# Optimization experiments

Measured on AMD Instinct MI355X. Metric: run time of the kernel, lower is better.

The kernel has to match this reference:

```python
import jax, jax.numpy as jnp
import numpy as np

MAX_DET = 100
IOU_THR = 0.5


def _iou_matrix(b):
    # b: [N,4] xyxy -> [N,N] pairwise IoU
    area = jnp.clip(b[:, 2] - b[:, 0], 0) * jnp.clip(b[:, 3] - b[:, 1], 0)
    lt = jnp.maximum(b[:, None, :2], b[None, :, :2])
    rb = jnp.minimum(b[:, None, 2:], b[None, :, 2:])
    wh = jnp.clip(rb - lt, 0)
    inter = wh[..., 0] * wh[..., 1]
    union = area[:, None] + area[None, :] - inter
    return inter / jnp.maximum(union, 1e-8)


def _batched_nms(boxes, scores, classes, iou_thr, max_out):
    # torchvision batched_nms semantics: offset boxes by class id so
    # boxes of different classes never overlap, then greedy NMS.
    n = boxes.shape[0]
    order = jnp.argsort(-scores)
    b = boxes[order]
    c = classes[order]
    off = c.astype(b.dtype) * (jnp.max(b) + 1.0)
    iou = _iou_matrix(b + off[:, None])  # [N,N]

    def body(valid, _):
        idx = jnp.argmax(valid)          # highest-score surviving candidate
        any_valid = jnp.any(valid)
        new_valid = valid & ~(iou[idx] > iou_thr)
        new_valid = new_valid.at[idx].set(False)
        sel = jnp.where(any_valid, order[idx], -1)
        return new_valid, sel

    _, sel = jax.lax.scan(body, jnp.ones(n, dtype=bool), None, length=max_out)
    return sel  # [max_out] indices into original order, -1 padded


def _detect_one(cls_o, box_o, idx, cls_ids, scale, size, anchor_boxes):
    a = anchor_boxes[idx]  # [N,4] yxyx
    yc_a = (a[:, 0] + a[:, 2]) * 0.5
    xc_a = (a[:, 1] + a[:, 3]) * 0.5
    ha = a[:, 2] - a[:, 0]
    wa = a[:, 3] - a[:, 1]
    box = box_o.astype(jnp.float32)
    ty, tx, th, tw = box[:, 0], box[:, 1], box[:, 2], box[:, 3]
    w = jnp.exp(tw) * wa
    h = jnp.exp(th) * ha
    yc = ty * ha + yc_a
    xc = tx * wa + xc_a
    boxes = jnp.stack([xc - w * 0.5, yc - h * 0.5, xc + w * 0.5, yc + h * 0.5], axis=1)
    # clip_boxes_xyxy with size = img_size / img_scale
    sz = jnp.concatenate([size, size]) / scale  # [4]
    boxes = jnp.minimum(jnp.clip(boxes, 0), sz[None, :])
    scores = jax.nn.sigmoid(cls_o[:, 0]).astype(jnp.float32)
    sel = _batched_nms(boxes, scores, cls_ids, IOU_THR, MAX_DET)
    safe = jnp.maximum(sel, 0)
    valid = (sel >= 0).astype(jnp.float32)[:, None]
    det = jnp.concatenate([
        boxes[safe] * scale,
        scores[safe][:, None],
        (cls_ids[safe] + 1).astype(jnp.float32)[:, None],
    ], axis=1)
    return det * valid  # zero-pad rows past num_det


def setup_inputs() -> dict:
    key = jax.random.key(0)
    ks = jax.random.split(key, 7)
    B, N, A, C = 8, 4096, 49104, 90
    cls_outputs = jax.random.normal(ks[0], (B, N, 1), jnp.float32)
    box_outputs = jax.random.normal(ks[1], (B, N, 4), jnp.float32) * 0.2
    indices = jax.random.randint(ks[2], (B, N), 0, A)
    classes = jax.random.randint(ks[3], (B, N), 0, C)
    # anchor boxes in yxyx, roughly covering a 512x512 image
    ctr = jax.random.uniform(ks[4], (A, 2), jnp.float32, 0.0, 512.0)
    hw = jax.random.uniform(ks[5], (A, 2), jnp.float32, 16.0, 128.0)
    anchor_boxes = jnp.concatenate([ctr - hw * 0.5, ctr + hw * 0.5], axis=1)
    img_scale = jax.random.uniform(ks[6], (B,), jnp.float32, 0.5, 1.5)
    img_size = jnp.full((B, 2), 512.0, jnp.float32)
    return dict(cls_outputs=cls_outputs, box_outputs=box_outputs,
                indices=indices, classes=classes, anchor_boxes=anchor_boxes,
                img_scale=img_scale, img_size=img_size)


def reference(cls_outputs, box_outputs, indices, classes, anchor_boxes, img_scale, img_size):
    f = jax.vmap(_detect_one, in_axes=(0, 0, 0, 0, 0, 0, None))
    return f(cls_outputs, box_outputs, indices, classes, img_scale, img_size, anchor_boxes)
```

## Files before the change

kernel.cpp:

```cpp
#include <hip/hip_runtime.h>
#include <stdint.h>

#define N_DET    4096
#define HALF     2048
#define MAX_DET  100
#define NTHREADS 1024
#define SORT_THREADS 512
#define DEC_THREADS 512
#define DEC_CHUNKS  8
#define IOU_THR  0.5f

typedef unsigned long long u64;

__device__ __forceinline__ float fadd(float a, float b) { return __fadd_rn(a, b); }
__device__ __forceinline__ float fsub(float a, float b) { return __fsub_rn(a, b); }
__device__ __forceinline__ float fmul(float a, float b) { return __fmul_rn(a, b); }

struct Box { float x1, y1, x2, y2; };

__device__ __forceinline__ Box decode_box(const float* __restrict__ box_b,
                                          const int*   __restrict__ idx_b,
                                          const float* __restrict__ anchors,
                                          int i, float sz0, float sz1)
{
    int ai = idx_b[i];
    float a0 = anchors[ai * 4 + 0];
    float a1 = anchors[ai * 4 + 1];
    float a2 = anchors[ai * 4 + 2];
    float a3 = anchors[ai * 4 + 3];
    float yc_a = fmul(fadd(a0, a2), 0.5f);
    float xc_a = fmul(fadd(a1, a3), 0.5f);
    float ha = fsub(a2, a0);
    float wa = fsub(a3, a1);
    float ty = box_b[i * 4 + 0];
    float tx = box_b[i * 4 + 1];
    float th = box_b[i * 4 + 2];
    float tw = box_b[i * 4 + 3];
    float we = fmul(expf(tw), wa);
    float he = fmul(expf(th), ha);
    float yc = fadd(fmul(ty, ha), yc_a);
    float xc = fadd(fmul(tx, wa), xc_a);
    Box r;
    r.x1 = fsub(xc, fmul(we, 0.5f));
    r.y1 = fsub(yc, fmul(he, 0.5f));
    r.x2 = fadd(xc, fmul(we, 0.5f));
    r.y2 = fadd(yc, fmul(he, 0.5f));
    r.x1 = fminf(fmaxf(r.x1, 0.f), sz0);
    r.y1 = fminf(fmaxf(r.y1, 0.f), sz1);
    r.x2 = fminf(fmaxf(r.x2, 0.f), sz0);
    r.y2 = fminf(fmaxf(r.y2, 0.f), sz1);
    return r;
}

__device__ __forceinline__ float sigmoidf_ref(float x)
{
    return __fdiv_rn(1.0f, __fadd_rn(1.0f, expf(-x)));
}

__device__ __forceinline__ bool iou_suppress(float hx1, float hy1, float hx2, float hy2, float har,
                                             float cx1, float cy1, float cx2, float cy2, float car)
{
    float lt0 = fmaxf(hx1, cx1);
    float lt1 = fmaxf(hy1, cy1);
    float rb0 = fminf(hx2, cx2);
    float rb1 = fminf(hy2, cy2);
    float w0 = fmaxf(fsub(rb0, lt0), 0.f);
    float w1 = fmaxf(fsub(rb1, lt1), 0.f);
    float inter = fmul(w0, w1);
    float uni = fsub(fadd(har, car), inter);
    float iou = __fdiv_rn(inter, fmaxf(uni, 1e-8f));
    return iou > IOU_THR;
}

__device__ __forceinline__ u64 shfl_xor_u64(u64 x, int mask)
{
    unsigned lo = (unsigned)x, hi = (unsigned)(x >> 32);
    lo = __shfl_xor(lo, mask, 64);
    hi = __shfl_xor(hi, mask, 64);
    return ((u64)hi << 32) | lo;
}

__device__ __forceinline__ void cex(u64& a, u64& b, bool desc)
{
    bool sw = desc ? (a < b) : (a > b);
    u64 ta = a, tb = b;
    a = sw ? tb : ta;
    b = sw ? ta : tb;
}

__device__ __forceinline__ void shuf_pass(u64 e[4], int d, bool desc, int l)
{
    bool lower = ((l & d) == 0);
    bool keepmax = (desc == lower);
    #pragma unroll
    for (int s = 0; s < 4; ++s) {
        u64 p = shfl_xor_u64(e[s], d);
        u64 mx = (e[s] > p) ? e[s] : p;
        u64 mn = (e[s] < p) ? e[s] : p;
        e[s] = keepmax ? mx : mn;
    }
}

__device__ __forceinline__ void shuf_pass2(u64 e[2], int d, int l)
{
    bool keepmax = ((l & d) == 0);
    #pragma unroll
    for (int s = 0; s < 2; ++s) {
        u64 p = shfl_xor_u64(e[s], d);
        u64 mx = (e[s] > p) ? e[s] : p;
        u64 mn = (e[s] < p) ? e[s] : p;
        e[s] = keepmax ? mx : mn;
    }
}

__global__ __launch_bounds__(DEC_THREADS)
void decode_kernel(const float* __restrict__ cls_outputs,
                   const float* __restrict__ box_outputs,
                   const int*   __restrict__ indices,
                   const float* __restrict__ anchors,
                   const float* __restrict__ img_scale,
                   const float* __restrict__ img_size,
                   float*       __restrict__ wmax,
                   u64*         __restrict__ wkeys,
                   float4*      __restrict__ wboxes)
{
    const int blk   = blockIdx.x;
    const int b     = blk / DEC_CHUNKS;
    const int chunk = blk % DEC_CHUNKS;
    const int i     = chunk * DEC_THREADS + threadIdx.x;

    const float* cls_b = cls_outputs + (size_t)b * N_DET;
    const float* box_b = box_outputs + (size_t)b * N_DET * 4;
    const int*   idx_b = indices + (size_t)b * N_DET;
    const float  scale = img_scale[b];
    const float  sz0   = __fdiv_rn(img_size[b * 2 + 0], scale);
    const float  sz1   = __fdiv_rn(img_size[b * 2 + 1], scale);

    Box r = decode_box(box_b, idx_b, anchors, i, sz0, sz1);
    float sc = sigmoidf_ref(cls_b[i]);

    wboxes[(size_t)b * N_DET + i] = make_float4(r.x1, r.y1, r.x2, r.y2);
    wkeys[(size_t)b * N_DET + i] =
        ((u64)__float_as_uint(sc) << 32) | (unsigned)(N_DET - 1 - i);

    float lmax = fmaxf(fmaxf(r.x1, r.y1), fmaxf(r.x2, r.y2));
    for (int o = 32; o; o >>= 1) lmax = fmaxf(lmax, __shfl_xor(lmax, o, 64));
    __shared__ float wred[8];
    if ((threadIdx.x & 63) == 0) wred[threadIdx.x >> 6] = lmax;
    __syncthreads();
    if (threadIdx.x == 0) {
        float m = wred[0];
        #pragma unroll
        for (int k = 1; k < 8; ++k) m = fmaxf(m, wred[k]);
        wmax[b * DEC_CHUNKS + chunk] = m;
    }
}

__global__ __launch_bounds__(SORT_THREADS, 1)
void sort_half_kernel(u64* __restrict__ wkeys)
{
    __shared__ u64 keys[HALF];
    u64* gk = wkeys + (size_t)blockIdx.x * HALF;
    const int t = threadIdx.x;
    const int l = t & 63;

    u64 e[4];
    #pragma unroll
    for (int s = 0; s < 4; ++s) e[s] = gk[4 * t + s];

    cex(e[0], e[1], true);
    cex(e[2], e[3], false);
    for (int k = 4; k <= 128; k <<= 1) {
        bool desc = (l & (k >> 2)) == 0;
        for (int j = k >> 1; j >= 4; j >>= 1) shuf_pass(e, j >> 2, desc, l);
        cex(e[0], e[2], desc); cex(e[1], e[3], desc);
        cex(e[0], e[1], desc); cex(e[2], e[3], desc);
    }
    {
        bool desc = ((t >> 6) & 1) == 0;
        for (int j = 128; j >= 4; j >>= 1) shuf_pass(e, j >> 2, desc, l);
        cex(e[0], e[2], desc); cex(e[1], e[3], desc);
        cex(e[0], e[1], desc); cex(e[2], e[3], desc);
    }
    #pragma unroll
    for (int s = 0; s < 4; ++s) keys[4 * t + s] = e[s];

    for (int k = 512; k <= HALF; k <<= 1) {
        for (int j = k >> 1; j >= 256; j >>= 1) {
            __syncthreads();
            #pragma unroll
            for (int vv = 0; vv < 2; ++vv) {
                int v = t + vv * SORT_THREADS;
                int i   = ((v & ~(j - 1)) << 1) | (v & (j - 1));
                int ixj = i | j;
                bool desc = ((i & k) == 0);
                u64 a = keys[i], c = keys[ixj];
                bool sw = desc ? (a < c) : (a > c);
                if (sw) { keys[i] = c; keys[ixj] = a; }
            }
        }
        __syncthreads();
        u64 f[4];
        #pragma unroll
        for (int s = 0; s < 4; ++s) f[s] = keys[4 * t + s];
        bool desc = (t & (k >> 2)) == 0;
        for (int j = 128; j >= 4; j >>= 1) shuf_pass(f, j >> 2, desc, l);
        cex(f[0], f[2], desc); cex(f[1], f[3], desc);
        cex(f[0], f[1], desc); cex(f[2], f[3], desc);
        #pragma unroll
        for (int s = 0; s < 4; ++s) keys[4 * t + s] = f[s];
    }
    __syncthreads();
    #pragma unroll
    for (int s = 0; s < 4; ++s) gk[4 * t + s] = keys[4 * t + s];
}

__global__ __launch_bounds__(NTHREADS, 1)
void scan_kernel(const int*    __restrict__ classes,
                 const float*  __restrict__ img_scale,
                 const float*  __restrict__ wmax,
                 const u64*    __restrict__ wkeys,
                 const float4* __restrict__ wboxes,
                 float*        __restrict__ out)
{
    __shared__ float4 bbox[64];
    __shared__ float  barr[64];
    __shared__ int    borig[64];
    __shared__ u64    bkey[64];
    __shared__ u64    extp[16];
    __shared__ unsigned Cplo[16][64];
    __shared__ unsigned Cphi[16][64];
    __shared__ int    sel[MAX_DET];
    __shared__ float  selsc[MAX_DET];
    __shared__ float4 hbox4[MAX_DET];
    __shared__ float  harr[MAX_DET];
    __shared__ int    sh_count;

    const int b = blockIdx.x;
    const int t = threadIdx.x;
    const int l = t & 63;

    const int*    cls_id_b = classes + (size_t)b * N_DET;
    const float   scale    = img_scale[b];
    const u64*    gA = wkeys + (size_t)b * N_DET;
    const u64*    gB = gA + HALF;
    const float4* wb = wboxes + (size_t)b * N_DET;

    float mm = wmax[b * DEC_CHUNKS + 0];
    #pragma unroll
    for (int k = 1; k < DEC_CHUNKS; ++k) mm = fmaxf(mm, wmax[b * DEC_CHUNKS + k]);
    const float M = fadd(mm, 1.0f);

    if (t < MAX_DET) sel[t] = -1;
    if (t == 0) sh_count = 0;
    __syncthreads();

    int pa = 0, pb = 0;
    const int j = t & 63;
    const int g = t >> 6;

    for (int c = 0; c < N_DET; c += 64) {
        int count = sh_count;
        if (count >= MAX_DET) break;

        if (t < 64) {
            u64 ee[2];
            if (l < 32) {
                int p0 = pa + 2 * l;
                ee[0] = (p0     < HALF) ? gA[p0]     : 0ull;
                ee[1] = (p0 + 1 < HALF) ? gA[p0 + 1] : 0ull;
            } else {
                int p  = 2 * (l - 32);
                int q0 = pb + 63 - p;
                ee[0] = (q0     < HALF) ? gB[q0]     : 0ull;
                ee[1] = (q0 - 1 < HALF && q0 - 1 >= 0) ? gB[q0 - 1] : 0ull;
            }
            shuf_pass2(ee, 32, l); shuf_pass2(ee, 16, l); shuf_pass2(ee, 8, l);
            shuf_pass2(ee, 4, l);  shuf_pass2(ee, 2, l);  shuf_pass2(ee, 1, l);
            cex(ee[0], ee[1], true);

            int orig0 = N_DET - 1 - (int)(unsigned)(ee[0] & 0xFFFFFFFFull);
            int orig1 = N_DET - 1 - (int)(unsigned)(ee[1] & 0xFFFFFFFFull);
            bool r0 = (l < 32) && (ee[0] != 0ull);
            bool r1 = (l < 32) && (ee[1] != 0ull);
            if (l < 32) {
                #pragma unroll
                for (int s = 0; s < 2; ++s) {
                    int  r    = 2 * l + s;
                    u64  key  = s ? ee[1] : ee[0];
                    int  orig = s ? orig1 : orig0;
                    bool ok   = s ? r1 : r0;
                    bkey[r] = key;
                    if (ok) {
                        float4 bb = wb[orig];
                        float off = fmul((float)cls_id_b[orig], M);
                        float x1 = fadd(bb.x, off), y1 = fadd(bb.y, off);
                        float x2 = fadd(bb.z, off), y2 = fadd(bb.w, off);
                        bbox[r] = make_float4(x1, y1, x2, y2);
                        barr[r] = fmul(fmaxf(fsub(x2, x1), 0.f), fmaxf(fsub(y2, y1), 0.f));
                        borig[r] = orig;
                    } else {
                        bbox[r] = make_float4(0.f, 0.f, 0.f, 0.f);
                        barr[r] = 0.f;
                        borig[r] = -1;
                    }
                }
            }
            u64 bR0 = __ballot(r0), bR1 = __ballot(r1);
            u64 bA0 = __ballot(r0 && (orig0 < HALF));
            u64 bA1 = __ballot(r1 && (orig1 < HALF));
            int real = __popcll(bR0) + __popcll(bR1);
            int aw   = __popcll(bA0) + __popcll(bA1);
            pa += aw;
            pb += real - aw;
        }
        __syncthreads();

        float4 c4  = bbox[j];
        float  car = barr[j];
        const bool valid = (borig[j] >= 0);

        bool sup = !valid;
        for (int k = g; k < count; k += 16) {
            float4 h4 = hbox4[k];
            sup = sup | iou_suppress(h4.x, h4.y, h4.z, h4.w, harr[k],
                                     c4.x, c4.y, c4.z, c4.w, car);
        }
        u64 bal = __ballot(sup ? 1 : 0);
        if ((t & 63) == 0) extp[g] = bal;

        unsigned cplo = 0, cphi = 0;
        for (int r = g + 1; r < 64; r += 16) {
            int q = j ^ r;
            float4 q4 = bbox[q];
            float qar = barr[q];
            bool hit = (q > j) & valid & (borig[q] >= 0) &
                       iou_suppress(c4.x, c4.y, c4.z, c4.w, car,
                                    q4.x, q4.y, q4.z, q4.w, qar);
            unsigned bit = hit ? 1u : 0u;
            if (q < 32) cplo |= bit << q; else cphi |= bit << (q - 32);
        }
        Cplo[g][j] = cplo;
        Cphi[g][j] = cphi;
        __syncthreads();

        if (t < 64) {
            const int lane = t;
            u64 ext = 0;
            #pragma unroll
            for (int gg = 0; gg < 16; ++gg) ext |= extp[gg];
            unsigned lo = 0, hi = 0;
            #pragma unroll
            for (int gg = 0; gg < 16; ++gg) { lo |= Cplo[gg][lane]; hi |= Cphi[gg][lane]; }
            u64 C = ((u64)hi << 32) | lo;
            u64 hasC = __ballot(C != 0ull);

            u64 alive = ~ext;
            u64 selmask = 0;
            int total = count;
            while (alive && total < MAX_DET) {
                int k = __ffsll(alive) - 1;
                selmask |= (1ull << k);
                alive &= ~(1ull << k);
                ++total;
                if ((hasC >> k) & 1ull) {
                    unsigned clo = __shfl((int)(unsigned)C, k, 64);
                    unsigned chi = __shfl((int)(unsigned)(C >> 32), k, 64);
                    alive &= ~(((u64)chi << 32) | clo);
                }
            }

            if ((selmask >> lane) & 1ull) {
                int p = count + __popcll(selmask & ((1ull << lane) - 1ull));
                hbox4[p] = bbox[lane];
                harr[p]  = barr[lane];
                sel[p]   = borig[lane];
                selsc[p] = __uint_as_float((unsigned)(bkey[lane] >> 32));
            }
            if (lane == 0) sh_count = total;
        }
        __syncthreads();
    }

    if (t >= 64) return;
    for (int r = t; r < MAX_DET; r += 64) {
        int sidx = sel[r];
        float* o = out + (size_t)b * MAX_DET * 6 + (size_t)r * 6;
        if (sidx < 0) {
            o[0] = 0.f; o[1] = 0.f; o[2] = 0.f; o[3] = 0.f; o[4] = 0.f; o[5] = 0.f;
        } else {
            float4 bb = wb[sidx];
            int c = cls_id_b[sidx];
            o[0] = fmul(bb.x, scale);
            o[1] = fmul(bb.y, scale);
            o[2] = fmul(bb.z, scale);
            o[3] = fmul(bb.w, scale);
            o[4] = selsc[r];
            o[5] = (float)(c + 1);
        }
    }
}

extern "C" void kernel_launch(void* const* d_in, const int* in_sizes, int n_in,
                              void* d_out, int out_size, void* d_ws, size_t ws_size,
                              hipStream_t stream)
{
    const float* cls_outputs = (const float*)d_in[0];
    const float* box_outputs = (const float*)d_in[1];
    const int*   indices     = (const int*)d_in[2];
    const int*   classes     = (const int*)d_in[3];
    const float* anchors     = (const float*)d_in[4];
    const float* img_scale   = (const float*)d_in[5];
    const float* img_size    = (const float*)d_in[6];
    float*       out         = (float*)d_out;

    const int B = in_sizes[5];

    char* wsb = (char*)d_ws;
    float*  wmax   = (float*)wsb;
    u64*    wkeys  = (u64*)(wsb + 1024);
    float4* wboxes = (float4*)(wsb + 1024 + (size_t)B * N_DET * sizeof(u64));

    decode_kernel<<<dim3(B * DEC_CHUNKS), dim3(DEC_THREADS), 0, stream>>>(
        cls_outputs, box_outputs, indices, anchors, img_scale, img_size,
        wmax, wkeys, wboxes);

    sort_half_kernel<<<dim3(B * 2), dim3(SORT_THREADS), 0, stream>>>(wkeys);

    scan_kernel<<<dim3(B), dim3(NTHREADS), 0, stream>>>(
        classes, img_scale, wmax, wkeys, wboxes, out);
}
```

Measured before the change: 41.41 us.

## Pre-merge top 512 sorted keys in LDS before the NMS scan loop

At the start of the scan kernel, the top 512 keys of each sorted half are loaded into shared memory and bitonic-merged in one block-wide step. The first eight 64-candidate chunks are then read straight from shared memory, replacing the per-chunk wave-level merge of global keys. The A/B read pointers are set from a ballot count so the old per-chunk merge path can take over after 512 candidates. The decode kernel is also split into more, smaller blocks. The trade-off is extra upfront work and barriers plus 8KB of shared memory, which is wasted if NMS finishes within a few chunks.

```diff
diff --git a/kernel.cpp b/kernel.cpp
--- a/kernel.cpp
+++ b/kernel.cpp
@@ -6,8 +6,8 @@
 #define MAX_DET  100
 #define NTHREADS 1024
 #define SORT_THREADS 512
-#define DEC_THREADS 512
-#define DEC_CHUNKS  8
+#define DEC_THREADS 256
+#define DEC_CHUNKS  16
 #define IOU_THR  0.5f
 
 typedef unsigned long long u64;
@@ -145,13 +145,13 @@
 
     float lmax = fmaxf(fmaxf(r.x1, r.y1), fmaxf(r.x2, r.y2));
     for (int o = 32; o; o >>= 1) lmax = fmaxf(lmax, __shfl_xor(lmax, o, 64));
-    __shared__ float wred[8];
+    __shared__ float wred[DEC_THREADS / 64];
     if ((threadIdx.x & 63) == 0) wred[threadIdx.x >> 6] = lmax;
     __syncthreads();
     if (threadIdx.x == 0) {
         float m = wred[0];
         #pragma unroll
-        for (int k = 1; k < 8; ++k) m = fmaxf(m, wred[k]);
+        for (int k = 1; k < DEC_THREADS / 64; ++k) m = fmaxf(m, wred[k]);
         wmax[b * DEC_CHUNKS + chunk] = m;
     }
 }
@@ -223,6 +223,8 @@
                  const float4* __restrict__ wboxes,
                  float*        __restrict__ out)
 {
+    __shared__ u64    mstream[1024];
+    __shared__ int    waveA[8];
     __shared__ float4 bbox[64];
     __shared__ float  barr[64];
     __shared__ int    borig[64];
@@ -251,11 +253,53 @@
     for (int k = 1; k < DEC_CHUNKS; ++k) mm = fmaxf(mm, wmax[b * DEC_CHUNKS + k]);
     const float M = fadd(mm, 1.0f);
 
+    if (t < 512) mstream[t] = gA[t];
+    else         mstream[t] = gB[511 - (t - 512)];
     if (t < MAX_DET) sel[t] = -1;
     if (t == 0) sh_count = 0;
     __syncthreads();
 
-    int pa = 0, pb = 0;
+    {
+        if (t < 512) {
+            u64 a = mstream[t], c = mstream[t + 512];
+            if (a < c) { mstream[t] = c; mstream[t + 512] = a; }
+        }
+        __syncthreads();
+        if (t < 512) {
+            int i   = ((t & ~255) << 1) | (t & 255);
+            int ixj = i | 256;
+            u64 a = mstream[i], c = mstream[ixj];
+            if (a < c) { mstream[i] = c; mstream[ixj] = a; }
+        }
+        __syncthreads();
+        if (t < 256) {
+            u64 f[4];
+            #pragma unroll
+            for (int s = 0; s < 4; ++s) f[s] = mstream[4 * t + s];
+            for (int j = 128; j >= 4; j >>= 1) shuf_pass(f, j >> 2, true, l);
+            cex(f[0], f[2], true); cex(f[1], f[3], true);
+            cex(f[0], f[1], true); cex(f[2], f[3], true);
+            #pragma unroll
+            for (int s = 0; s < 4; ++s) mstream[4 * t + s] = f[s];
+        }
+        __syncthreads();
+    }
+
+    {
+        bool isA = false;
+        if (t < 512) {
+            int orig = N_DET - 1 - (int)(unsigned)(mstream[t] & 0xFFFFFFFFull);
+            isA = (orig < HALF);
+        }
+        u64 bal = __ballot(isA ? 1 : 0);
+        if ((t & 63) == 0 && (t >> 6) < 8) waveA[t >> 6] = __popcll(bal);
+        __syncthreads();
+    }
+    int pa = 0;
+    #pragma unroll
+    for (int w = 0; w < 8; ++w) pa += waveA[w];
+    int pb = 512 - pa;
+
     const int j = t & 63;
     const int g = t >> 6;
 
@@ -263,56 +307,70 @@
         int count = sh_count;
         if (count >= MAX_DET) break;
 
-        if (t < 64) {
-            u64 ee[2];
-            if (l < 32) {
-                int p0 = pa + 2 * l;
-                ee[0] = (p0     < HALF) ? gA[p0]     : 0ull;
-                ee[1] = (p0 + 1 < HALF) ? gA[p0 + 1] : 0ull;
-            } else {
-                int p  = 2 * (l - 32);
-                int q0 = pb + 63 - p;
-                ee[0] = (q0     < HALF) ? gB[q0]     : 0ull;
-                ee[1] = (q0 - 1 < HALF && q0 - 1 >= 0) ? gB[q0 - 1] : 0ull;
+        if (c + 64 <= 512) {
+            if (t < 64) {
+                u64 key = mstream[c + t];
+                int orig = N_DET - 1 - (int)(unsigned)(key & 0xFFFFFFFFull);
+                bkey[t] = key; borig[t] = orig;
+                float4 bb = wb[orig];
+                float off = fmul((float)cls_id_b[orig], M);
+                float x1 = fadd(bb.x, off), y1 = fadd(bb.y, off);
+                float x2 = fadd(bb.z, off), y2 = fadd(bb.w, off);
+                bbox[t] = make_float4(x1, y1, x2, y2);
+                barr[t] = fmul(fmaxf(fsub(x2, x1), 0.f), fmaxf(fsub(y2, y1), 0.f));
             }
-            shuf_pass2(ee, 32, l); shuf_pass2(ee, 16, l); shuf_pass2(ee, 8, l);
-            shuf_pass2(ee, 4, l);  shuf_pass2(ee, 2, l);  shuf_pass2(ee, 1, l);
-            cex(ee[0], ee[1], true);
-
-            int orig0 = N_DET - 1 - (int)(unsigned)(ee[0] & 0xFFFFFFFFull);
-            int orig1 = N_DET - 1 - (int)(unsigned)(ee[1] & 0xFFFFFFFFull);
-            bool r0 = (l < 32) && (ee[0] != 0ull);
-            bool r1 = (l < 32) && (ee[1] != 0ull);
-            if (l < 32) {
-                #pragma unroll
-                for (int s = 0; s < 2; ++s) {
-                    int  r    = 2 * l + s;
-                    u64  key  = s ? ee[1] : ee[0];
-                    int  orig = s ? orig1 : orig0;
-                    bool ok   = s ? r1 : r0;
-                    bkey[r] = key;
-                    if (ok) {
-                        float4 bb = wb[orig];
-                        float off = fmul((float)cls_id_b[orig], M);
-                        float x1 = fadd(bb.x, off), y1 = fadd(bb.y, off);
-                        float x2 = fadd(bb.z, off), y2 = fadd(bb.w, off);
-                        bbox[r] = make_float4(x1, y1, x2, y2);
-                        barr[r] = fmul(fmaxf(fsub(x2, x1), 0.f), fmaxf(fsub(y2, y1), 0.f));
-                        borig[r] = orig;
-                    } else {
-                        bbox[r] = make_float4(0.f, 0.f, 0.f, 0.f);
-                        barr[r] = 0.f;
-                        borig[r] = -1;
+        } else {
+            if (t < 64) {
+                u64 ee[2];
+                if (l < 32) {
+                    int p0 = pa + 2 * l;
+                    ee[0] = (p0     < HALF) ? gA[p0]     : 0ull;
+                    ee[1] = (p0 + 1 < HALF) ? gA[p0 + 1] : 0ull;
+                } else {
+                    int p  = 2 * (l - 32);
+                    int q0 = pb + 63 - p;
+                    ee[0] = (q0     < HALF) ? gB[q0]     : 0ull;
+                    ee[1] = (q0 - 1 < HALF && q0 - 1 >= 0) ? gB[q0 - 1] : 0ull;
+                }
+                shuf_pass2(ee, 32, l); shuf_pass2(ee, 16, l); shuf_pass2(ee, 8, l);
+                shuf_pass2(ee, 4, l);  shuf_pass2(ee, 2, l);  shuf_pass2(ee, 1, l);
+                cex(ee[0], ee[1], true);
+
+                int orig0 = N_DET - 1 - (int)(unsigned)(ee[0] & 0xFFFFFFFFull);
+                int orig1 = N_DET - 1 - (int)(unsigned)(ee[1] & 0xFFFFFFFFull);
+                bool r0 = (l < 32) && (ee[0] != 0ull);
+                bool r1 = (l < 32) && (ee[1] != 0ull);
+                if (l < 32) {
+                    #pragma unroll
+                    for (int s = 0; s < 2; ++s) {
+                        int  r    = 2 * l + s;
+                        u64  key  = s ? ee[1] : ee[0];
+                        int  orig = s ? orig1 : orig0;
+                        bool ok   = s ? r1 : r0;
+                        bkey[r] = key;
+                        if (ok) {
+                            float4 bb = wb[orig];
+                            float off = fmul((float)cls_id_b[orig], M);
+                            float x1 = fadd(bb.x, off), y1 = fadd(bb.y, off);
+                            float x2 = fadd(bb.z, off), y2 = fadd(bb.w, off);
+                            bbox[r] = make_float4(x1, y1, x2, y2);
+                            barr[r] = fmul(fmaxf(fsub(x2, x1), 0.f), fmaxf(fsub(y2, y1), 0.f));
+                            borig[r] = orig;
+                        } else {
+                            bbox[r] = make_float4(0.f, 0.f, 0.f, 0.f);
+                            barr[r] = 0.f;
+                            borig[r] = -1;
+                        }
                     }
                 }
+                u64 bR0 = __ballot(r0), bR1 = __ballot(r1);
+                u64 bA0 = __ballot(r0 && (orig0 < HALF));
+                u64 bA1 = __ballot(r1 && (orig1 < HALF));
+                int real = __popcll(bR0) + __popcll(bR1);
+                int aw   = __popcll(bA0) + __popcll(bA1);
+                pa += aw;
+                pb += real - aw;
             }
-            u64 bR0 = __ballot(r0), bR1 = __ballot(r1);
-            u64 bA0 = __ballot(r0 && (orig0 < HALF));
-            u64 bA1 = __ballot(r1 && (orig1 < HALF));
-            int real = __popcll(bR0) + __popcll(bR1);
-            int aw   = __popcll(bA0) + __popcll(bA1);
-            pa += aw;
-            pb += real - aw;
         }
         __syncthreads();
 
```

Measured after the change: 40.12 us. 1.03x faster.
